# Optimization experiments

Hardware: AMD Instinct MI355X
Metric: run time of the kernel (lower is better)

The kernel has to match this reference:

```python
import jax, jax.numpy as jnp
import numpy as np

M_INST = 64   # num_instances (labels 1..64; 0 = background)
L_ANCH = 8    # anchors per instance
C_DIM = 256   # anchor_dim == embed dim (num_mapping_layers=0, num_heads=1)
B, H, W = 8, 64, 64


def setup_inputs() -> dict:
    key = jax.random.key(0)
    ks = jax.random.split(key, 7)
    s = 1.0 / np.sqrt(C_DIM)
    return {
        "anchors": jax.random.normal(ks[0], (M_INST, L_ANCH, C_DIM), jnp.float32),
        "features": jax.random.normal(ks[1], (B, H, W, C_DIM), jnp.float32),
        "instances_in_view": jax.random.randint(ks[2], (B, H, W), 0, M_INST + 1, jnp.int32),
        # nn.MultiheadAttention packed in-projection and out-projection params
        "in_proj_w": jax.random.normal(ks[3], (3 * C_DIM, C_DIM), jnp.float32) * s,
        "in_proj_b": jax.random.normal(ks[4], (3 * C_DIM,), jnp.float32) * s,
        "out_w": jax.random.normal(ks[5], (C_DIM, C_DIM), jnp.float32) * s,
        "out_b": jax.random.normal(ks[6], (C_DIM,), jnp.float32) * s,
    }


def reference(anchors, features, instances_in_view, in_proj_w, in_proj_b, out_w, out_b):
    # Cross-attention anchor_type, Identity maps (num_mapping_layers=0, num_heads=1).
    # Each pixel (query) attends to the L anchors of its instance; padding in the
    # original pad_sequence pipeline never affects non-pad queries, so the
    # gather/pack -> MHA -> unmap -> residual-add pipeline reduces to per-pixel math.
    C = anchors.shape[-1]
    Wq, Wk, Wv = in_proj_w[:C], in_proj_w[C:2 * C], in_proj_w[2 * C:]
    bq, bk, bv = in_proj_b[:C], in_proj_b[C:2 * C], in_proj_b[2 * C:]

    # Project keys/values once per instance: (M, L, C)
    K = jnp.einsum('mlc,dc->mld', anchors, Wk) + bk
    V = jnp.einsum('mlc,dc->mld', anchors, Wv) + bv

    Bsz, Hh, Ww, _ = features.shape
    f = features.reshape(-1, C)                       # (N, C)
    lab = instances_in_view.reshape(-1)               # (N,) labels 0..M
    idx = jnp.maximum(lab - 1, 0)                     # anchor row per pixel

    q = f @ Wq.T + bq                                 # (N, C)
    Kg = K[idx]                                       # (N, L, C) irregular gather
    Vg = V[idx]                                       # (N, L, C)

    scale = 1.0 / np.sqrt(C).astype(np.float32)
    scores = jnp.einsum('nc,nlc->nl', q, Kg) * scale  # (N, L)
    attn = jax.nn.softmax(scores, axis=-1)
    o = jnp.einsum('nl,nlc->nc', attn, Vg)            # (N, C)
    o = o @ out_w.T + out_b                           # MHA out_proj

    # background (label 0) pixels get zero anchor feature; residual add
    o = jnp.where((lab > 0)[:, None], o, jnp.zeros((), o.dtype))
    out = f + o
    return out.reshape(Bsz, Hh, Ww, C)
```

## Files before the change

kernel.cpp:

```cpp
#include <hip/hip_runtime.h>
#include <stdint.h>

#define C_DIM   256
#define L_ANCH  8
#define M_INST  64
#define NPIX    32768
#define LDSTR   264
#define TSTR    80
#define GUSTR   512

typedef __attribute__((ext_vector_type(8))) short  short8;
typedef __attribute__((ext_vector_type(4))) float  float4v;

__device__ __forceinline__ float bf2f(unsigned short b) {
    union { unsigned u; float f; } x; x.u = ((unsigned)b) << 16; return x.f;
}
__device__ __forceinline__ unsigned short f2bf(float f) {
    union { unsigned u; float f; } x; x.f = f;
    unsigned u = x.u;
    return (unsigned short)((u + 0x7FFFu + ((u >> 16) & 1u)) >> 16);
}
__device__ __forceinline__ ushort4 f4bf(float4 f) {
    ushort4 v; v.x = f2bf(f.x); v.y = f2bf(f.y); v.z = f2bf(f.z); v.w = f2bf(f.w);
    return v;
}
__device__ __forceinline__ short8 f8bf(float4 a, float4 b) {
    union { short8 v; ushort4 q[2]; } u;
    u.q[0] = f4bf(a); u.q[1] = f4bf(b);
    return u.v;
}
__device__ __forceinline__ void bfx2(unsigned u, float& lo, float& hi) {
    union { unsigned u; float f; } a, b;
    a.u = u << 16; b.u = u & 0xffff0000u;
    lo = a.f; hi = b.f;
}

__global__ __launch_bounds__(256) void prep1_kernel(
    const float* __restrict__ anchors, const float* __restrict__ in_proj_w,
    const float* __restrict__ in_proj_b,
    unsigned short* __restrict__ Kb, unsigned short* __restrict__ Vb,
    unsigned short* __restrict__ WqT)
{
    __shared__ unsigned short Abuf[32 * LDSTR];
    __shared__ unsigned short Ttile[64 * TSTR];
    const int b = blockIdx.x, t = threadIdx.x;

    if (b >= 64) {
        const int tidx = b - 64;
        const int r0 = (tidx >> 2) * 64, c0 = (tidx & 3) * 64;
#pragma unroll
        for (int i = 0; i < 4; ++i) {
            int id = t + i * 256;
            int row = id >> 4, c4 = id & 15;
            float4 f = *(const float4*)&in_proj_w[(size_t)(r0 + row) * C_DIM + c0 + c4 * 4];
            Ttile[(c4 * 4 + 0) * TSTR + row] = f2bf(f.x);
            Ttile[(c4 * 4 + 1) * TSTR + row] = f2bf(f.y);
            Ttile[(c4 * 4 + 2) * TSTR + row] = f2bf(f.z);
            Ttile[(c4 * 4 + 3) * TSTR + row] = f2bf(f.w);
        }
        __syncthreads();
#pragma unroll
        for (int i = 0; i < 2; ++i) {
            int id = t + i * 256;
            int cc = id >> 3, ch = id & 7;
            *(short8*)&WqT[(size_t)(c0 + cc) * C_DIM + r0 + ch * 8] =
                *(const short8*)&Ttile[cc * TSTR + ch * 8];
        }
        return;
    }

    const int mat = b >> 5, tile = (b >> 1) & 15, half = b & 1;
    const int m0 = tile * 32;
#pragma unroll
    for (int i = 0; i < 8; ++i) {
        int id = t + i * 256;
        int row = id >> 6, c4 = id & 63;
        float4 f = *((const float4*)(anchors + (size_t)(m0 + row) * C_DIM) + c4);
        *(ushort4*)&Abuf[row * LDSTR + c4 * 4] = f4bf(f);
    }
    __syncthreads();

    const int wave = t >> 6, lane = t & 63, r16 = lane & 15, quad = lane >> 4;
    const int colbase = half * 128 + wave * 32;
    const int wbase = C_DIM + mat * C_DIM + colbase;

    float4v acc[2][2];
#pragma unroll
    for (int mt = 0; mt < 2; ++mt)
#pragma unroll
        for (int nt = 0; nt < 2; ++nt)
#pragma unroll
            for (int r = 0; r < 4; ++r) acc[mt][nt][r] = 0.f;

#pragma unroll 2
    for (int ks = 0; ks < 8; ++ks) {
        const int c0 = ks * 32 + quad * 8;
        short8 afr[2], bfr[2];
#pragma unroll
        for (int mt = 0; mt < 2; ++mt)
            afr[mt] = *(const short8*)&Abuf[(mt * 16 + r16) * LDSTR + c0];
#pragma unroll
        for (int nt = 0; nt < 2; ++nt) {
            const float* wrow = in_proj_w + (size_t)(wbase + nt * 16 + r16) * C_DIM + c0;
            bfr[nt] = f8bf(*(const float4*)wrow, *(const float4*)(wrow + 4));
        }
#pragma unroll
        for (int mt = 0; mt < 2; ++mt)
#pragma unroll
            for (int nt = 0; nt < 2; ++nt)
                acc[mt][nt] = __builtin_amdgcn_mfma_f32_16x16x32_bf16(
                    afr[mt], bfr[nt], acc[mt][nt], 0, 0, 0);
    }

    unsigned short* dst = mat ? Vb : Kb;
#pragma unroll
    for (int nt = 0; nt < 2; ++nt) {
        const int col = colbase + nt * 16 + r16;
        const float bias = in_proj_b[C_DIM + mat * C_DIM + col];
#pragma unroll
        for (int mt = 0; mt < 2; ++mt)
#pragma unroll
            for (int r = 0; r < 4; ++r) {
                int row = m0 + mt * 16 + quad * 4 + r;
                dst[(size_t)row * C_DIM + col] = f2bf(acc[mt][nt][r] + bias);
            }
    }
}

__global__ __launch_bounds__(256) void prep2_kernel(
    const unsigned short* __restrict__ Kb, const unsigned short* __restrict__ Vb,
    const unsigned short* __restrict__ WqT, const float* __restrict__ out_w,
    const float* __restrict__ in_proj_b,
    unsigned short* __restrict__ GU, float* __restrict__ g0)
{
    const int b = blockIdx.x, t = threadIdx.x;
    const int isG = (b < 32) ? 1 : 0;
    const int tile = (b >> 1) & 15, half = b & 1;
    const int m0 = tile * 32;
    const unsigned short* src = isG ? Kb : Vb;
    const int ucol = isG ? 0 : 256;

    const int wave = t >> 6, lane = t & 63, r16 = lane & 15, quad = lane >> 4;

    if (isG && half == 0) {
        const int grow = t >> 3, gs = t & 7;
        const unsigned short* kr = Kb + (size_t)(m0 + grow) * C_DIM + gs * 32;
        float gp = 0.f;
#pragma unroll
        for (int c8 = 0; c8 < 4; ++c8) {
            short8 kv = *(const short8*)(kr + c8 * 8);
            const float* bp = in_proj_b + gs * 32 + c8 * 8;
#pragma unroll
            for (int j = 0; j < 8; ++j)
                gp += bf2f((unsigned short)kv[j]) * bp[j];
        }
        gp += __shfl_down(gp, 1);
        gp += __shfl_down(gp, 2);
        gp += __shfl_down(gp, 4);
        if (gs == 0) g0[m0 + grow] = gp;
    }

    const int colbase = half * 128 + wave * 32;

    float4v acc[2][2];
#pragma unroll
    for (int mt = 0; mt < 2; ++mt)
#pragma unroll
        for (int nt = 0; nt < 2; ++nt)
#pragma unroll
            for (int r = 0; r < 4; ++r) acc[mt][nt][r] = 0.f;

#pragma unroll 2
    for (int ks = 0; ks < 8; ++ks) {
        const int c0 = ks * 32 + quad * 8;
        short8 afr[2], bfr[2];
#pragma unroll
        for (int mt = 0; mt < 2; ++mt)
            afr[mt] = *(const short8*)&src[(size_t)(m0 + mt * 16 + r16) * C_DIM + c0];
#pragma unroll
        for (int nt = 0; nt < 2; ++nt) {
            const int wr = colbase + nt * 16 + r16;
            if (isG) {
                bfr[nt] = *(const short8*)&WqT[(size_t)wr * C_DIM + c0];
            } else {
                const float* wp = out_w + (size_t)wr * C_DIM + c0;
                bfr[nt] = f8bf(*(const float4*)wp, *(const float4*)(wp + 4));
            }
        }
#pragma unroll
        for (int mt = 0; mt < 2; ++mt)
#pragma unroll
            for (int nt = 0; nt < 2; ++nt)
                acc[mt][nt] = __builtin_amdgcn_mfma_f32_16x16x32_bf16(
                    afr[mt], bfr[nt], acc[mt][nt], 0, 0, 0);
    }

#pragma unroll
    for (int nt = 0; nt < 2; ++nt) {
        const int col = colbase + nt * 16 + r16;
#pragma unroll
        for (int mt = 0; mt < 2; ++mt)
#pragma unroll
            for (int r = 0; r < 4; ++r) {
                int row = m0 + mt * 16 + quad * 4 + r;
                GU[(size_t)row * GUSTR + ucol + col] = f2bf(acc[mt][nt][r]);
            }
    }
}

__global__ __launch_bounds__(256) void gather_kernel(
    const float* __restrict__ features, const int* __restrict__ inst,
    const float* __restrict__ out_b,
    const unsigned short* __restrict__ GU, const float* __restrict__ g0,
    float* __restrict__ out)
{
    const int t = threadIdx.x;
    const int p = t >> 4, s = t & 15;
    const int n = blockIdx.x * 16 + p;
    const int lab = inst[n];
    const int m = max(lab - 1, 0);
    const unsigned short* GUp = GU + (size_t)m * (L_ANCH * GUSTR) + s * 16;

    float fr[16];
    const float4* fp = (const float4*)(features + (size_t)n * C_DIM + s * 16);
#pragma unroll
    for (int i = 0; i < 4; ++i) *(float4*)&fr[i * 4] = fp[i];

    float sc[L_ANCH];
#pragma unroll
    for (int l = 0; l < L_ANCH; ++l) {
        const uint4* rp = (const uint4*)(GUp + (size_t)l * GUSTR);
        uint4 w0 = rp[0], w1 = rp[1];
        float a = 0.f, lo, hi;
        bfx2(w0.x, lo, hi); a += lo * fr[0]  + hi * fr[1];
        bfx2(w0.y, lo, hi); a += lo * fr[2]  + hi * fr[3];
        bfx2(w0.z, lo, hi); a += lo * fr[4]  + hi * fr[5];
        bfx2(w0.w, lo, hi); a += lo * fr[6]  + hi * fr[7];
        bfx2(w1.x, lo, hi); a += lo * fr[8]  + hi * fr[9];
        bfx2(w1.y, lo, hi); a += lo * fr[10] + hi * fr[11];
        bfx2(w1.z, lo, hi); a += lo * fr[12] + hi * fr[13];
        bfx2(w1.w, lo, hi); a += lo * fr[14] + hi * fr[15];
        sc[l] = a;
    }

    const float4 g0a = *(const float4*)&g0[m * L_ANCH];
    const float4 g0b = *(const float4*)&g0[m * L_ANCH + 4];
    const float gb[L_ANCH] = {g0a.x, g0a.y, g0a.z, g0a.w, g0b.x, g0b.y, g0b.z, g0b.w};

    float mx = -1e30f;
#pragma unroll
    for (int l = 0; l < L_ANCH; ++l) {
        float v = sc[l];
        v += __shfl_xor(v, 1);
        v += __shfl_xor(v, 2);
        v += __shfl_xor(v, 4);
        v += __shfl_xor(v, 8);
        v = (v + gb[l]) * 0.0625f;
        sc[l] = v;
        mx = fmaxf(mx, v);
    }
    float sum = 0.f;
#pragma unroll
    for (int l = 0; l < L_ANCH; ++l) { sc[l] = __expf(sc[l] - mx); sum += sc[l]; }
    const float inv = 1.f / sum;

    float y[16];
#pragma unroll
    for (int c = 0; c < 16; ++c) y[c] = 0.f;
#pragma unroll
    for (int l = 0; l < L_ANCH; ++l) {
        const float av = sc[l] * inv;
        const uint4* up = (const uint4*)(GUp + (size_t)l * GUSTR + 256);
        uint4 u0 = up[0], u1 = up[1];
        float lo, hi;
        bfx2(u0.x, lo, hi); y[0]  += av * lo; y[1]  += av * hi;
        bfx2(u0.y, lo, hi); y[2]  += av * lo; y[3]  += av * hi;
        bfx2(u0.z, lo, hi); y[4]  += av * lo; y[5]  += av * hi;
        bfx2(u0.w, lo, hi); y[6]  += av * lo; y[7]  += av * hi;
        bfx2(u1.x, lo, hi); y[8]  += av * lo; y[9]  += av * hi;
        bfx2(u1.y, lo, hi); y[10] += av * lo; y[11] += av * hi;
        bfx2(u1.z, lo, hi); y[12] += av * lo; y[13] += av * hi;
        bfx2(u1.w, lo, hi); y[14] += av * lo; y[15] += av * hi;
    }

    const float fm = (lab > 0) ? 1.f : 0.f;
    float4* op = (float4*)(out + (size_t)n * C_DIM + s * 16);
    const float4* obp = (const float4*)(out_b + s * 16);
#pragma unroll
    for (int i = 0; i < 4; ++i) {
        float4 ob = obp[i];
        float4 o;
        o.x = fr[i * 4 + 0] + fm * (y[i * 4 + 0] + ob.x);
        o.y = fr[i * 4 + 1] + fm * (y[i * 4 + 1] + ob.y);
        o.z = fr[i * 4 + 2] + fm * (y[i * 4 + 2] + ob.z);
        o.w = fr[i * 4 + 3] + fm * (y[i * 4 + 3] + ob.w);
        op[i] = o;
    }
}

extern "C" void kernel_launch(void* const* d_in, const int* in_sizes, int n_in,
                              void* d_out, int out_size, void* d_ws, size_t ws_size,
                              hipStream_t stream) {
    const float* anchors   = (const float*)d_in[0];
    const float* features  = (const float*)d_in[1];
    const int*   inst      = (const int*)d_in[2];
    const float* in_proj_w = (const float*)d_in[3];
    const float* in_proj_b = (const float*)d_in[4];
    const float* out_w     = (const float*)d_in[5];
    const float* out_b     = (const float*)d_in[6];
    float* out = (float*)d_out;

    unsigned short* Kb  = (unsigned short*)d_ws;
    unsigned short* Vb  = Kb  + M_INST * L_ANCH * C_DIM;
    unsigned short* WqT = Vb  + M_INST * L_ANCH * C_DIM;
    unsigned short* GU  = WqT + C_DIM * C_DIM;
    float*          g0  = (float*)(GU + M_INST * L_ANCH * GUSTR);

    prep1_kernel<<<80, 256, 0, stream>>>(anchors, in_proj_w, in_proj_b, Kb, Vb, WqT);
    prep2_kernel<<<64, 256, 0, stream>>>(Kb, Vb, WqT, out_w, in_proj_b, GU, g0);
    gather_kernel<<<NPIX / 16, 256, 0, stream>>>(features, inst, out_b, GU, g0, out);
}
```

Baseline: 128.1 us.

## Fuse the two prep kernels into one, keeping projected K/V in LDS

Merges prep1 and prep2 into a single prep kernel. Each block now computes all 256 columns of its K or V tile into shared memory and then runs the second GEMM (against Wq or out_w) from that LDS tile. This drops one kernel launch and the global round-trip for K, V and the transposed Wq. In exchange, each pair of half-blocks recomputes the full first projection, and Wq is read with strided scalar column loads plus on-the-fly bf16 conversion instead of from a pre-transposed copy.

```diff
diff --git a/kernel.cpp b/kernel.cpp
--- a/kernel.cpp
+++ b/kernel.cpp
@@ -6,7 +6,6 @@
 #define M_INST  64
 #define NPIX    32768
 #define LDSTR   264
-#define TSTR    80
 #define GUSTR   512
 
 typedef __attribute__((ext_vector_type(8))) short  short8;
@@ -35,42 +34,19 @@
     lo = a.f; hi = b.f;
 }
 
-__global__ __launch_bounds__(256) void prep1_kernel(
+__global__ __launch_bounds__(256) void prep_kernel(
     const float* __restrict__ anchors, const float* __restrict__ in_proj_w,
-    const float* __restrict__ in_proj_b,
-    unsigned short* __restrict__ Kb, unsigned short* __restrict__ Vb,
-    unsigned short* __restrict__ WqT)
+    const float* __restrict__ in_proj_b, const float* __restrict__ out_w,
+    unsigned short* __restrict__ GU, float* __restrict__ g0)
 {
     __shared__ unsigned short Abuf[32 * LDSTR];
-    __shared__ unsigned short Ttile[64 * TSTR];
+    __shared__ unsigned short Tbuf[32 * LDSTR];
     const int b = blockIdx.x, t = threadIdx.x;
-
-    if (b >= 64) {
-        const int tidx = b - 64;
-        const int r0 = (tidx >> 2) * 64, c0 = (tidx & 3) * 64;
-#pragma unroll
-        for (int i = 0; i < 4; ++i) {
-            int id = t + i * 256;
-            int row = id >> 4, c4 = id & 15;
-            float4 f = *(const float4*)&in_proj_w[(size_t)(r0 + row) * C_DIM + c0 + c4 * 4];
-            Ttile[(c4 * 4 + 0) * TSTR + row] = f2bf(f.x);
-            Ttile[(c4 * 4 + 1) * TSTR + row] = f2bf(f.y);
-            Ttile[(c4 * 4 + 2) * TSTR + row] = f2bf(f.z);
-            Ttile[(c4 * 4 + 3) * TSTR + row] = f2bf(f.w);
-        }
-        __syncthreads();
-#pragma unroll
-        for (int i = 0; i < 2; ++i) {
-            int id = t + i * 256;
-            int cc = id >> 3, ch = id & 7;
-            *(short8*)&WqT[(size_t)(c0 + cc) * C_DIM + r0 + ch * 8] =
-                *(const short8*)&Ttile[cc * TSTR + ch * 8];
-        }
-        return;
-    }
-
-    const int mat = b >> 5, tile = (b >> 1) & 15, half = b & 1;
+    const int isG = (b < 32) ? 1 : 0;
+    const int tile = (b >> 1) & 15, half = b & 1;
     const int m0 = tile * 32;
+    const int ucol = isG ? 0 : 256;
+
 #pragma unroll
     for (int i = 0; i < 8; ++i) {
         int id = t + i * 256;
@@ -81,16 +57,75 @@
     __syncthreads();
 
     const int wave = t >> 6, lane = t & 63, r16 = lane & 15, quad = lane >> 4;
-    const int colbase = half * 128 + wave * 32;
-    const int wbase = C_DIM + mat * C_DIM + colbase;
-
-    float4v acc[2][2];
+
+    const int w1base = C_DIM + (isG ? 0 : C_DIM);
+    const int cb1 = wave * 64;
+
+    float4v acc1[2][4];
 #pragma unroll
     for (int mt = 0; mt < 2; ++mt)
 #pragma unroll
+        for (int nt = 0; nt < 4; ++nt)
+#pragma unroll
+            for (int r = 0; r < 4; ++r) acc1[mt][nt][r] = 0.f;
+
+#pragma unroll 2
+    for (int ks = 0; ks < 8; ++ks) {
+        const int c0 = ks * 32 + quad * 8;
+        short8 afr[2], bfr[4];
+#pragma unroll
+        for (int mt = 0; mt < 2; ++mt)
+            afr[mt] = *(const short8*)&Abuf[(mt * 16 + r16) * LDSTR + c0];
+#pragma unroll
+        for (int nt = 0; nt < 4; ++nt) {
+            const float* wrow = in_proj_w + (size_t)(w1base + cb1 + nt * 16 + r16) * C_DIM + c0;
+            bfr[nt] = f8bf(*(const float4*)wrow, *(const float4*)(wrow + 4));
+        }
+#pragma unroll
+        for (int mt = 0; mt < 2; ++mt)
+#pragma unroll
+            for (int nt = 0; nt < 4; ++nt)
+                acc1[mt][nt] = __builtin_amdgcn_mfma_f32_16x16x32_bf16(
+                    afr[mt], bfr[nt], acc1[mt][nt], 0, 0, 0);
+    }
+
+#pragma unroll
+    for (int nt = 0; nt < 4; ++nt) {
+        const int col = cb1 + nt * 16 + r16;
+        const float bias = in_proj_b[w1base + col];
+#pragma unroll
+        for (int mt = 0; mt < 2; ++mt)
+#pragma unroll
+            for (int r = 0; r < 4; ++r) {
+                int row = mt * 16 + quad * 4 + r;
+                Tbuf[row * LDSTR + col] = f2bf(acc1[mt][nt][r] + bias);
+            }
+    }
+    __syncthreads();
+
+    if (isG && half == 0) {
+        const int grow = t >> 3, gs = t & 7;
+        const unsigned short* tr = &Tbuf[grow * LDSTR + gs * 32];
+        const float* bp = in_proj_b + gs * 32;
+        float gp = 0.f;
+#pragma unroll
+        for (int c = 0; c < 32; ++c)
+            gp += bf2f(tr[c]) * bp[c];
+        gp += __shfl_down(gp, 1);
+        gp += __shfl_down(gp, 2);
+        gp += __shfl_down(gp, 4);
+        if (gs == 0) g0[m0 + grow] = gp;
+    }
+
+    const int cb2 = half * 128 + wave * 32;
+
+    float4v acc2[2][2];
+#pragma unroll
+    for (int mt = 0; mt < 2; ++mt)
+#pragma unroll
         for (int nt = 0; nt < 2; ++nt)
 #pragma unroll
-            for (int r = 0; r < 4; ++r) acc[mt][nt][r] = 0.f;
+            for (int r = 0; r < 4; ++r) acc2[mt][nt][r] = 0.f;
 
 #pragma unroll 2
     for (int ks = 0; ks < 8; ++ks) {
@@ -98,92 +133,18 @@
         short8 afr[2], bfr[2];
 #pragma unroll
         for (int mt = 0; mt < 2; ++mt)
-            afr[mt] = *(const short8*)&Abuf[(mt * 16 + r16) * LDSTR + c0];
+            afr[mt] = *(const short8*)&Tbuf[(mt * 16 + r16) * LDSTR + c0];
 #pragma unroll
         for (int nt = 0; nt < 2; ++nt) {
-            const float* wrow = in_proj_w + (size_t)(wbase + nt * 16 + r16) * C_DIM + c0;
-            bfr[nt] = f8bf(*(const float4*)wrow, *(const float4*)(wrow + 4));
-        }
-#pragma unroll
-        for (int mt = 0; mt < 2; ++mt)
-#pragma unroll
-            for (int nt = 0; nt < 2; ++nt)
-                acc[mt][nt] = __builtin_amdgcn_mfma_f32_16x16x32_bf16(
-                    afr[mt], bfr[nt], acc[mt][nt], 0, 0, 0);
-    }
-
-    unsigned short* dst = mat ? Vb : Kb;
-#pragma unroll
-    for (int nt = 0; nt < 2; ++nt) {
-        const int col = colbase + nt * 16 + r16;
-        const float bias = in_proj_b[C_DIM + mat * C_DIM + col];
-#pragma unroll
-        for (int mt = 0; mt < 2; ++mt)
-#pragma unroll
-            for (int r = 0; r < 4; ++r) {
-                int row = m0 + mt * 16 + quad * 4 + r;
-                dst[(size_t)row * C_DIM + col] = f2bf(acc[mt][nt][r] + bias);
-            }
-    }
-}
-
-__global__ __launch_bounds__(256) void prep2_kernel(
-    const unsigned short* __restrict__ Kb, const unsigned short* __restrict__ Vb,
-    const unsigned short* __restrict__ WqT, const float* __restrict__ out_w,
-    const float* __restrict__ in_proj_b,
-    unsigned short* __restrict__ GU, float* __restrict__ g0)
-{
-    const int b = blockIdx.x, t = threadIdx.x;
-    const int isG = (b < 32) ? 1 : 0;
-    const int tile = (b >> 1) & 15, half = b & 1;
-    const int m0 = tile * 32;
-    const unsigned short* src = isG ? Kb : Vb;
-    const int ucol = isG ? 0 : 256;
-
-    const int wave = t >> 6, lane = t & 63, r16 = lane & 15, quad = lane >> 4;
-
-    if (isG && half == 0) {
-        const int grow = t >> 3, gs = t & 7;
-        const unsigned short* kr = Kb + (size_t)(m0 + grow) * C_DIM + gs * 32;
-        float gp = 0.f;
-#pragma unroll
-        for (int c8 = 0; c8 < 4; ++c8) {
-            short8 kv = *(const short8*)(kr + c8 * 8);
-            const float* bp = in_proj_b + gs * 32 + c8 * 8;
-#pragma unroll
-            for (int j = 0; j < 8; ++j)
-                gp += bf2f((unsigned short)kv[j]) * bp[j];
-        }
-        gp += __shfl_down(gp, 1);
-        gp += __shfl_down(gp, 2);
-        gp += __shfl_down(gp, 4);
-        if (gs == 0) g0[m0 + grow] = gp;
-    }
-
-    const int colbase = half * 128 + wave * 32;
-
-    float4v acc[2][2];
-#pragma unroll
-    for (int mt = 0; mt < 2; ++mt)
-#pragma unroll
-        for (int nt = 0; nt < 2; ++nt)
-#pragma unroll
-            for (int r = 0; r < 4; ++r) acc[mt][nt][r] = 0.f;
-
-#pragma unroll 2
-    for (int ks = 0; ks < 8; ++ks) {
-        const int c0 = ks * 32 + quad * 8;
-        short8 afr[2], bfr[2];
-#pragma unroll
-        for (int mt = 0; mt < 2; ++mt)
-            afr[mt] = *(const short8*)&src[(size_t)(m0 + mt * 16 + r16) * C_DIM + c0];
-#pragma unroll
-        for (int nt = 0; nt < 2; ++nt) {
-            const int wr = colbase + nt * 16 + r16;
+            const int col = cb2 + nt * 16 + r16;
             if (isG) {
-                bfr[nt] = *(const short8*)&WqT[(size_t)wr * C_DIM + c0];
+                unsigned short tmp[8];
+#pragma unroll
+                for (int j = 0; j < 8; ++j)
+                    tmp[j] = f2bf(in_proj_w[(size_t)(c0 + j) * C_DIM + col]);
+                bfr[nt] = *(const short8*)tmp;
             } else {
-                const float* wp = out_w + (size_t)wr * C_DIM + c0;
+                const float* wp = out_w + (size_t)col * C_DIM + c0;
                 bfr[nt] = f8bf(*(const float4*)wp, *(const float4*)(wp + 4));
             }
         }
@@ -191,19 +152,19 @@
         for (int mt = 0; mt < 2; ++mt)
 #pragma unroll
             for (int nt = 0; nt < 2; ++nt)
-                acc[mt][nt] = __builtin_amdgcn_mfma_f32_16x16x32_bf16(
-                    afr[mt], bfr[nt], acc[mt][nt], 0, 0, 0);
+                acc2[mt][nt] = __builtin_amdgcn_mfma_f32_16x16x32_bf16(
+                    afr[mt], bfr[nt], acc2[mt][nt], 0, 0, 0);
     }
 
 #pragma unroll
     for (int nt = 0; nt < 2; ++nt) {
-        const int col = colbase + nt * 16 + r16;
+        const int col = cb2 + nt * 16 + r16;
 #pragma unroll
         for (int mt = 0; mt < 2; ++mt)
 #pragma unroll
             for (int r = 0; r < 4; ++r) {
                 int row = m0 + mt * 16 + quad * 4 + r;
-                GU[(size_t)row * GUSTR + ucol + col] = f2bf(acc[mt][nt][r]);
+                GU[(size_t)row * GUSTR + ucol + col] = f2bf(acc2[mt][nt][r]);
             }
     }
 }
@@ -310,13 +271,9 @@
     const float* out_b     = (const float*)d_in[6];
     float* out = (float*)d_out;
 
-    unsigned short* Kb  = (unsigned short*)d_ws;
-    unsigned short* Vb  = Kb  + M_INST * L_ANCH * C_DIM;
-    unsigned short* WqT = Vb  + M_INST * L_ANCH * C_DIM;
-    unsigned short* GU  = WqT + C_DIM * C_DIM;
-    float*          g0  = (float*)(GU + M_INST * L_ANCH * GUSTR);
-
-    prep1_kernel<<<80, 256, 0, stream>>>(anchors, in_proj_w, in_proj_b, Kb, Vb, WqT);
-    prep2_kernel<<<64, 256, 0, stream>>>(Kb, Vb, WqT, out_w, in_proj_b, GU, g0);
+    unsigned short* GU = (unsigned short*)d_ws;
+    float*          g0 = (float*)(GU + M_INST * L_ANCH * GUSTR);
+
+    prep_kernel<<<64, 256, 0, stream>>>(anchors, in_proj_w, in_proj_b, out_w, GU, g0);
     gather_kernel<<<NPIX / 16, 256, 0, stream>>>(features, inst, out_b, GU, g0, out);
 }
```

New measurement: 134.3 us. 1.05x slower.
